# Performance work log

Hardware: AMD Instinct MI355X
Metric: run time of the kernel (lower is better)

Reference implementation:

```python
import jax, jax.numpy as jnp
import numpy as np

EMBED_DIM = 768
HEAD_SIZE = 64

def setup_inputs() -> dict:
    key = jax.random.key(0)
    k1, k2, k3, k4 = jax.random.split(key, 4)
    x = jax.random.normal(k1, (4, 4096, EMBED_DIM), dtype=jnp.float32)
    # nn.Linear(E, H, bias=False) weights, stored as [E, H] for y = x @ W
    scale = 1.0 / np.sqrt(EMBED_DIM)
    Wk = jax.random.uniform(k2, (EMBED_DIM, HEAD_SIZE), jnp.float32, -scale, scale)
    Wq = jax.random.uniform(k3, (EMBED_DIM, HEAD_SIZE), jnp.float32, -scale, scale)
    Wv = jax.random.uniform(k4, (EMBED_DIM, HEAD_SIZE), jnp.float32, -scale, scale)
    return {"x": x, "Wk": Wk, "Wq": Wq, "Wv": Wv}

def reference(x, Wk, Wq, Wv):
    # x: [B, S, E]
    E = x.shape[2]
    K = jnp.einsum("bse,eh->bsh", x, Wk)  # [B, S, H]
    Q = jnp.einsum("bse,eh->bsh", x, Wq)
    V = jnp.einsum("bse,eh->bsh", x, Wv)
    # NOTE: original scales by embedding_dim**0.5, not head_size**0.5
    A = jnp.einsum("bqh,bkh->bqk", Q, K) / jnp.sqrt(jnp.asarray(E, x.dtype))
    A = jax.nn.softmax(A, axis=-1)
    # dropout is inference-mode identity
    return jnp.einsum("bqk,bkh->bqh", A, V)
```

## Files before the change

kernel.cpp:

```cpp
#include <hip/hip_runtime.h>

typedef __attribute__((ext_vector_type(8))) short short8;
typedef __attribute__((ext_vector_type(4))) short short4v;
typedef __attribute__((ext_vector_type(4))) float float4v;

__device__ __forceinline__ short f2bf(float f) {
    union { float f; unsigned u; } v; v.f = f;
    return (short)((v.u + 0x7fffu + ((v.u >> 16) & 1u)) >> 16);
}

__device__ __forceinline__ float fast_exp2(float x) {
#if __has_builtin(__builtin_amdgcn_exp2f)
    return __builtin_amdgcn_exp2f(x);
#else
    return exp2f(x);
#endif
}

__device__ __forceinline__ unsigned cvt_pk_bf16(float lo, float hi) {
    unsigned r;
    asm("v_cvt_pk_bf16_f32 %0, %1, %2" : "=v"(r) : "v"(lo), "v"(hi));
    return r;
}

__global__ void wtrans_kernel(const float* __restrict__ Wk, const float* __restrict__ Wq,
                              const float* __restrict__ Wv, short* __restrict__ Wt3T) {
    int idx = blockIdx.x * 256 + threadIdx.x;
    int p = idx / 12288;
    int rem = idx - p * 12288;
    int kstep = rem / 512;
    int r2 = rem - kstep * 512;
    int lane = r2 >> 3, i = r2 & 7;
    int quad = lane >> 4, l16 = lane & 15;
    int j = p >> 2, nt = p & 3;
    int n = nt * 16 + l16;
    int k = kstep * 32 + quad * 8 + i;
    const float* W = (j == 0) ? Wq : (j == 1 ? Wk : Wv);
    float scale = (j == 0) ? 0.05205877f : 1.0f;
    Wt3T[idx] = f2bf(W[k * 64 + n] * scale);
}

__global__ __launch_bounds__(256, 4) void proj_kernel(
    const float* __restrict__ x, const short* __restrict__ Wt3T,
    short* __restrict__ Qs, short* __restrict__ Kb, short* __restrict__ Vtr)
{
    __shared__ alignas(16) int Abuf[3][256];
    __shared__ alignas(16) short sm[16 * 72];
    const int tid = threadIdx.x;
    const int wave = tid >> 6, lane = tid & 63, quad = lane >> 4, l16 = lane & 15;
    const int m0 = blockIdx.x * 16;
    const int p0 = wave * 3;

    const int xrow = tid >> 4, xcol = (tid & 15) * 2;
    const float* xp = x + (size_t)(m0 + xrow) * 768 + xcol;
    const int aidx = xrow * 16 + (tid & 15);
    const short* wt0 = Wt3T + (size_t)(p0 * 24) * 512 + lane * 8;

    float4v acc[3];
#pragma unroll
    for (int t = 0; t < 3; ++t) acc[t] = (float4v){0.f, 0.f, 0.f, 0.f};

    {
        float2 u = *(const float2*)xp;
        Abuf[0][aidx] = ((unsigned short)f2bf(u.x)) | ((unsigned)f2bf(u.y) << 16);
    }
    short8 Wc0 = *(const short8*)(wt0);
    short8 Wc1 = *(const short8*)(wt0 + 12288);
    short8 Wc2 = *(const short8*)(wt0 + 24576);
    float2 Xn = *(const float2*)(xp + 32);
    __syncthreads();

#pragma unroll
    for (int it = 0; it < 24; ++it) {
        short8 Wn0, Wn1, Wn2;
        float2 Xn2;
        if (it < 23) {
            const short* wn = wt0 + (it + 1) * 512;
            Wn0 = *(const short8*)(wn);
            Wn1 = *(const short8*)(wn + 12288);
            Wn2 = *(const short8*)(wn + 24576);
        }
        if (it < 22) Xn2 = *(const float2*)(xp + (it + 2) * 32);

        short8 a = *(const short8*)((const short*)Abuf[it % 3] + l16 * 32 + quad * 8);
        acc[0] = __builtin_amdgcn_mfma_f32_16x16x32_bf16(a, Wc0, acc[0], 0, 0, 0);
        acc[1] = __builtin_amdgcn_mfma_f32_16x16x32_bf16(a, Wc1, acc[1], 0, 0, 0);
        acc[2] = __builtin_amdgcn_mfma_f32_16x16x32_bf16(a, Wc2, acc[2], 0, 0, 0);

        if (it < 23)
            Abuf[(it + 1) % 3][aidx] = ((unsigned short)f2bf(Xn.x)) | ((unsigned)f2bf(Xn.y) << 16);
        Xn = Xn2;
        Wc0 = Wn0; Wc1 = Wn1; Wc2 = Wn2;
        __syncthreads();
    }

#pragma unroll
    for (int t = 0; t < 3; ++t) {
        const int p = p0 + t, j = p >> 2, nt = p & 3;
        if (j < 2) {
            short* dst = (j == 0) ? Qs : Kb;
#pragma unroll
            for (int r = 0; r < 4; ++r)
                dst[(size_t)(m0 + quad * 4 + r) * 64 + nt * 16 + l16] = f2bf(acc[t][r]);
        } else {
#pragma unroll
            for (int r = 0; r < 4; ++r)
                sm[(quad * 4 + r) * 72 + nt * 16 + l16] = f2bf(acc[t][r]);
        }
    }
    __syncthreads();
    {
        const int h = tid >> 2, si = (tid & 3) * 4;
        const int b = m0 >> 12, s0 = m0 & 4095;
        const int sb = s0 + si;
        const int jb = (sb & ~63) | (sb & 0x23) | ((sb & 0x0C) << 1) | ((sb & 0x10) >> 2);
        short4v tmp;
#pragma unroll
        for (int i = 0; i < 4; ++i) tmp[i] = sm[(si + i) * 72 + h];
        *(short4v*)(Vtr + (size_t)(b * 64 + h) * 4096 + jb) = tmp;
    }
}

__global__ __launch_bounds__(256, 1) void attn_kernel(
    const short* __restrict__ Qs, const short* __restrict__ Kb, const short* __restrict__ Vt,
    float* __restrict__ Opart, float* __restrict__ Ll, int kv_len)
{
    __shared__ alignas(16) short Kl[2][64 * 72];
    __shared__ alignas(16) short Vl[2][64 * 72];

    const int tid = threadIdx.x;
    const int wave = tid >> 6, lane = tid & 63, quad = lane >> 4, l16 = lane & 15;
    const int qt = blockIdx.x, b = blockIdx.y, sp = blockIdx.z;
    const int q0 = qt * 256;
    const int bS = b * 4096;
    const int kv0 = sp * kv_len;

    short8 qb[4][2];
#pragma unroll
    for (int ntq = 0; ntq < 4; ++ntq)
#pragma unroll
        for (int ks = 0; ks < 2; ++ks)
            qb[ntq][ks] = *(const short8*)(Qs + (size_t)(bS + q0 + wave * 64 + ntq * 16 + l16) * 64 + ks * 32 + quad * 8);

    float4v o[4][4];
#pragma unroll
    for (int ntq = 0; ntq < 4; ++ntq)
#pragma unroll
        for (int nt = 0; nt < 4; ++nt) o[ntq][nt] = (float4v){0.f, 0.f, 0.f, 0.f};
    float rs[4] = {0.f, 0.f, 0.f, 0.f};

    const int sr = tid >> 2, sc = (tid & 3) * 16;

    const short* ksrc0 = Kb + (size_t)(bS + kv0 + sr) * 64 + sc;
    const short* vsrc0 = Vt + (size_t)(b * 64 + sr) * 4096 + kv0 + sc;

    const int ntiles = kv_len >> 6;

    short8 kr0 = *(const short8*)ksrc0;
    short8 kr1 = *(const short8*)(ksrc0 + 8);
    short8 vr0 = *(const short8*)vsrc0;
    short8 vr1 = *(const short8*)(vsrc0 + 8);
    *(short8*)&Kl[0][sr * 72 + sc]     = kr0;
    *(short8*)&Kl[0][sr * 72 + sc + 8] = kr1;
    *(short8*)&Vl[0][sr * 72 + sc]     = vr0;
    *(short8*)&Vl[0][sr * 72 + sc + 8] = vr1;
    if (ntiles > 1) {
        const short* kn = ksrc0 + (size_t)4096;
        kr0 = *(const short8*)kn;
        kr1 = *(const short8*)(kn + 8);
        const short* vn = vsrc0 + 64;
        vr0 = *(const short8*)vn;
        vr1 = *(const short8*)(vn + 8);
    }
    __syncthreads();

    for (int t = 0; t < ntiles; ++t) {
        const int c = t & 1;
        const short* klc = &Kl[c][0];
        const short* vlc = &Vl[c][0];

        union { unsigned u[8]; short8 h[2]; } pa0, pa1, pa2, pa3;
#pragma unroll
        for (int mtk = 0; mtk < 4; ++mtk) {
            short8 k0 = *(const short8*)&klc[(mtk * 16 + l16) * 72 + quad * 8];
            short8 k1 = *(const short8*)&klc[(mtk * 16 + l16) * 72 + 32 + quad * 8];
#define QK_NTQ(PA, NTQ)                                                          \
            {                                                                    \
                float4v s = (float4v){0.f, 0.f, 0.f, 0.f};                       \
                __builtin_amdgcn_s_setprio(1);                                   \
                s = __builtin_amdgcn_mfma_f32_16x16x32_bf16(k0, qb[NTQ][0], s, 0, 0, 0); \
                s = __builtin_amdgcn_mfma_f32_16x16x32_bf16(k1, qb[NTQ][1], s, 0, 0, 0); \
                __builtin_amdgcn_s_setprio(0);                                   \
                float e0 = fast_exp2(s[0]), e1 = fast_exp2(s[1]);                \
                float e2 = fast_exp2(s[2]), e3 = fast_exp2(s[3]);                \
                rs[NTQ] += (e0 + e1) + (e2 + e3);                                \
                PA.u[mtk * 2]     = cvt_pk_bf16(e0, e1);                         \
                PA.u[mtk * 2 + 1] = cvt_pk_bf16(e2, e3);                         \
            }
            QK_NTQ(pa0, 0)
            QK_NTQ(pa1, 1)
            QK_NTQ(pa2, 2)
            QK_NTQ(pa3, 3)
#undef QK_NTQ
        }

#pragma unroll
        for (int ks = 0; ks < 2; ++ks) {
            short8 bf[4];
#pragma unroll
            for (int nt = 0; nt < 4; ++nt)
                bf[nt] = *(const short8*)&vlc[(nt * 16 + l16) * 72 + ks * 32 + quad * 8];
            __builtin_amdgcn_s_setprio(1);
#pragma unroll
            for (int nt = 0; nt < 4; ++nt)
                o[0][nt] = __builtin_amdgcn_mfma_f32_16x16x32_bf16(pa0.h[ks], bf[nt], o[0][nt], 0, 0, 0);
#pragma unroll
            for (int nt = 0; nt < 4; ++nt)
                o[1][nt] = __builtin_amdgcn_mfma_f32_16x16x32_bf16(pa1.h[ks], bf[nt], o[1][nt], 0, 0, 0);
#pragma unroll
            for (int nt = 0; nt < 4; ++nt)
                o[2][nt] = __builtin_amdgcn_mfma_f32_16x16x32_bf16(pa2.h[ks], bf[nt], o[2][nt], 0, 0, 0);
#pragma unroll
            for (int nt = 0; nt < 4; ++nt)
                o[3][nt] = __builtin_amdgcn_mfma_f32_16x16x32_bf16(pa3.h[ks], bf[nt], o[3][nt], 0, 0, 0);
            __builtin_amdgcn_s_setprio(0);
        }

        if (t + 1 < ntiles) {
            short* kd = &Kl[c ^ 1][0];
            short* vd = &Vl[c ^ 1][0];
            *(short8*)&kd[sr * 72 + sc]     = kr0;
            *(short8*)&kd[sr * 72 + sc + 8] = kr1;
            *(short8*)&vd[sr * 72 + sc]     = vr0;
            *(short8*)&vd[sr * 72 + sc + 8] = vr1;
        }
        if (t + 2 < ntiles) {
            const short* kn = ksrc0 + (size_t)(t + 2) * 4096;
            kr0 = *(const short8*)kn;
            kr1 = *(const short8*)(kn + 8);
            const short* vn = vsrc0 + (t + 2) * 64;
            vr0 = *(const short8*)vn;
            vr1 = *(const short8*)(vn + 8);
        }
        __syncthreads();
    }

#pragma unroll
    for (int ntq = 0; ntq < 4; ++ntq) {
        rs[ntq] += __shfl_xor(rs[ntq], 16);
        rs[ntq] += __shfl_xor(rs[ntq], 32);
    }

#pragma unroll
    for (int ntq = 0; ntq < 4; ++ntq) {
#pragma unroll
        for (int nt = 0; nt < 4; ++nt)
#pragma unroll
            for (int r = 0; r < 4; ++r) {
                int qrow = q0 + wave * 64 + ntq * 16 + quad * 4 + r;
                Opart[((size_t)sp * 16384 + bS + qrow) * 64 + nt * 16 + l16] = o[ntq][nt][r];
            }
        if (quad == 0)
            Ll[(size_t)sp * 16384 + bS + q0 + wave * 64 + ntq * 16 + l16] = rs[ntq];
    }
}

__global__ void combine_kernel(const float* __restrict__ Opart, const float* __restrict__ Ll,
                               float* __restrict__ out, int nsplit) {
    int idx = blockIdx.x * 256 + threadIdx.x;
    int q = idx >> 6;
    float den = 0.f, num = 0.f;
    for (int s = 0; s < nsplit; ++s) {
        den += Ll[s * 16384 + q];
        num += Opart[(size_t)s * 1048576 + idx];
    }
    out[idx] = num / den;
}

extern "C" void kernel_launch(void* const* d_in, const int* in_sizes, int n_in,
                              void* d_out, int out_size, void* d_ws, size_t ws_size,
                              hipStream_t stream) {
    const float* x  = (const float*)d_in[0];
    const float* Wk = (const float*)d_in[1];
    const float* Wq = (const float*)d_in[2];
    const float* Wv = (const float*)d_in[3];
    float* out = (float*)d_out;

    char* w = (char*)d_ws;
    size_t off = 0;
    auto take = [&](size_t bytes) -> void* {
        void* p = w + off;
        off = (off + bytes + 255) & ~(size_t)255;
        return p;
    };
    short* Qs  = (short*)take((size_t)16384 * 64 * 2);
    short* Kb  = (short*)take((size_t)16384 * 64 * 2);
    short* Vt  = (short*)take((size_t)16384 * 64 * 2);
    short* Wt3 = (short*)take((size_t)3 * 64 * 768 * 2);

    size_t base = off;
    int nsplit = 4;
    while (nsplit > 1) {
        size_t need = base + (((size_t)nsplit * 16384 * 4 + 255) & ~(size_t)255)
                      + (size_t)nsplit * 16384 * 64 * 4 + 512;
        if (need <= ws_size) break;
        nsplit >>= 1;
    }
    float* Ll    = (float*)take((size_t)nsplit * 16384 * 4);
    float* Opart = (float*)take((size_t)nsplit * 16384 * 64 * 4);

    wtrans_kernel<<<576, 256, 0, stream>>>(Wk, Wq, Wv, Wt3);
    proj_kernel<<<1024, 256, 0, stream>>>(x, Wt3, Qs, Kb, Vt);
    dim3 ag(16, 4, nsplit);
    attn_kernel<<<ag, 256, 0, stream>>>(Qs, Kb, Vt, Opart, Ll, 4096 / nsplit);
    combine_kernel<<<4096, 256, 0, stream>>>(Opart, Ll, out, nsplit);
}
```

Baseline: 140.0 us.

## Load K/V fragments directly from global into registers, drop LDS staging

The attention kernel no longer stages K and V tiles through double-buffered shared memory with barriers. Each wave now loads its MFMA operand fragments straight from global memory into registers, prefetching the next tile during compute. Launch bounds are raised to 2 blocks per CU and the KV split count goes from 4 to 8 to add blocks. Each wave now fetches the full K/V tiles itself, so global/L2 traffic rises about fourfold, and the larger partial-output buffer makes the combine step costlier.

```diff
diff --git a/kernel.cpp b/kernel.cpp
--- a/kernel.cpp
+++ b/kernel.cpp
@@ -121,13 +121,10 @@
     }
 }
 
-__global__ __launch_bounds__(256, 1) void attn_kernel(
+__global__ __launch_bounds__(256, 2) void attn_kernel(
     const short* __restrict__ Qs, const short* __restrict__ Kb, const short* __restrict__ Vt,
     float* __restrict__ Opart, float* __restrict__ Ll, int kv_len)
 {
-    __shared__ alignas(16) short Kl[2][64 * 72];
-    __shared__ alignas(16) short Vl[2][64 * 72];
-
     const int tid = threadIdx.x;
     const int wave = tid >> 6, lane = tid & 63, quad = lane >> 4, l16 = lane & 15;
     const int qt = blockIdx.x, b = blockIdx.y, sp = blockIdx.z;
@@ -149,41 +146,29 @@
         for (int nt = 0; nt < 4; ++nt) o[ntq][nt] = (float4v){0.f, 0.f, 0.f, 0.f};
     float rs[4] = {0.f, 0.f, 0.f, 0.f};
 
-    const int sr = tid >> 2, sc = (tid & 3) * 16;
-
-    const short* ksrc0 = Kb + (size_t)(bS + kv0 + sr) * 64 + sc;
-    const short* vsrc0 = Vt + (size_t)(b * 64 + sr) * 4096 + kv0 + sc;
+    const short* kp = Kb + (size_t)(bS + kv0 + l16) * 64 + quad * 8;
+    const short* vp = Vt + (size_t)(b * 64 + l16) * 4096 + kv0 + quad * 8;
 
     const int ntiles = kv_len >> 6;
 
-    short8 kr0 = *(const short8*)ksrc0;
-    short8 kr1 = *(const short8*)(ksrc0 + 8);
-    short8 vr0 = *(const short8*)vsrc0;
-    short8 vr1 = *(const short8*)(vsrc0 + 8);
-    *(short8*)&Kl[0][sr * 72 + sc]     = kr0;
-    *(short8*)&Kl[0][sr * 72 + sc + 8] = kr1;
-    *(short8*)&Vl[0][sr * 72 + sc]     = vr0;
-    *(short8*)&Vl[0][sr * 72 + sc + 8] = vr1;
-    if (ntiles > 1) {
-        const short* kn = ksrc0 + (size_t)4096;
-        kr0 = *(const short8*)kn;
-        kr1 = *(const short8*)(kn + 8);
-        const short* vn = vsrc0 + 64;
-        vr0 = *(const short8*)vn;
-        vr1 = *(const short8*)(vn + 8);
-    }
-    __syncthreads();
+    short8 ka[4], kc[4], va[4], vb[4];
+#pragma unroll
+    for (int mtk = 0; mtk < 4; ++mtk) {
+        ka[mtk] = *(const short8*)(kp + mtk * 1024);
+        kc[mtk] = *(const short8*)(kp + mtk * 1024 + 32);
+    }
+#pragma unroll
+    for (int nt = 0; nt < 4; ++nt) {
+        va[nt] = *(const short8*)(vp + (size_t)nt * 65536);
+        vb[nt] = *(const short8*)(vp + (size_t)nt * 65536 + 32);
+    }
 
     for (int t = 0; t < ntiles; ++t) {
-        const int c = t & 1;
-        const short* klc = &Kl[c][0];
-        const short* vlc = &Vl[c][0];
-
         union { unsigned u[8]; short8 h[2]; } pa0, pa1, pa2, pa3;
 #pragma unroll
         for (int mtk = 0; mtk < 4; ++mtk) {
-            short8 k0 = *(const short8*)&klc[(mtk * 16 + l16) * 72 + quad * 8];
-            short8 k1 = *(const short8*)&klc[(mtk * 16 + l16) * 72 + 32 + quad * 8];
+            short8 k0 = ka[mtk];
+            short8 k1 = kc[mtk];
 #define QK_NTQ(PA, NTQ)                                                          \
             {                                                                    \
                 float4v s = (float4v){0.f, 0.f, 0.f, 0.f};                       \
@@ -204,45 +189,37 @@
 #undef QK_NTQ
         }
 
+        if (t + 1 < ntiles) {
+            const short* kn = kp + (size_t)(t + 1) * 4096;
+#pragma unroll
+            for (int mtk = 0; mtk < 4; ++mtk) {
+                ka[mtk] = *(const short8*)(kn + mtk * 1024);
+                kc[mtk] = *(const short8*)(kn + mtk * 1024 + 32);
+            }
+        }
+
 #pragma unroll
         for (int ks = 0; ks < 2; ++ks) {
-            short8 bf[4];
-#pragma unroll
-            for (int nt = 0; nt < 4; ++nt)
-                bf[nt] = *(const short8*)&vlc[(nt * 16 + l16) * 72 + ks * 32 + quad * 8];
             __builtin_amdgcn_s_setprio(1);
 #pragma unroll
-            for (int nt = 0; nt < 4; ++nt)
-                o[0][nt] = __builtin_amdgcn_mfma_f32_16x16x32_bf16(pa0.h[ks], bf[nt], o[0][nt], 0, 0, 0);
-#pragma unroll
-            for (int nt = 0; nt < 4; ++nt)
-                o[1][nt] = __builtin_amdgcn_mfma_f32_16x16x32_bf16(pa1.h[ks], bf[nt], o[1][nt], 0, 0, 0);
-#pragma unroll
-            for (int nt = 0; nt < 4; ++nt)
-                o[2][nt] = __builtin_amdgcn_mfma_f32_16x16x32_bf16(pa2.h[ks], bf[nt], o[2][nt], 0, 0, 0);
-#pragma unroll
-            for (int nt = 0; nt < 4; ++nt)
-                o[3][nt] = __builtin_amdgcn_mfma_f32_16x16x32_bf16(pa3.h[ks], bf[nt], o[3][nt], 0, 0, 0);
+            for (int nt = 0; nt < 4; ++nt) {
+                short8 bf = (ks == 0) ? va[nt] : vb[nt];
+                o[0][nt] = __builtin_amdgcn_mfma_f32_16x16x32_bf16(pa0.h[ks], bf, o[0][nt], 0, 0, 0);
+                o[1][nt] = __builtin_amdgcn_mfma_f32_16x16x32_bf16(pa1.h[ks], bf, o[1][nt], 0, 0, 0);
+                o[2][nt] = __builtin_amdgcn_mfma_f32_16x16x32_bf16(pa2.h[ks], bf, o[2][nt], 0, 0, 0);
+                o[3][nt] = __builtin_amdgcn_mfma_f32_16x16x32_bf16(pa3.h[ks], bf, o[3][nt], 0, 0, 0);
+            }
             __builtin_amdgcn_s_setprio(0);
         }
 
         if (t + 1 < ntiles) {
-            short* kd = &Kl[c ^ 1][0];
-            short* vd = &Vl[c ^ 1][0];
-            *(short8*)&kd[sr * 72 + sc]     = kr0;
-            *(short8*)&kd[sr * 72 + sc + 8] = kr1;
-            *(short8*)&vd[sr * 72 + sc]     = vr0;
-            *(short8*)&vd[sr * 72 + sc + 8] = vr1;
-        }
-        if (t + 2 < ntiles) {
-            const short* kn = ksrc0 + (size_t)(t + 2) * 4096;
-            kr0 = *(const short8*)kn;
-            kr1 = *(const short8*)(kn + 8);
-            const short* vn = vsrc0 + (t + 2) * 64;
-            vr0 = *(const short8*)vn;
-            vr1 = *(const short8*)(vn + 8);
-        }
-        __syncthreads();
+            const short* vn = vp + (t + 1) * 64;
+#pragma unroll
+            for (int nt = 0; nt < 4; ++nt) {
+                va[nt] = *(const short8*)(vn + (size_t)nt * 65536);
+                vb[nt] = *(const short8*)(vn + (size_t)nt * 65536 + 32);
+            }
+        }
     }
 
 #pragma unroll
@@ -299,7 +276,7 @@
     short* Wt3 = (short*)take((size_t)3 * 64 * 768 * 2);
 
     size_t base = off;
-    int nsplit = 4;
+    int nsplit = 8;
     while (nsplit > 1) {
         size_t need = base + (((size_t)nsplit * 16384 * 4 + 255) & ~(size_t)255)
                       + (size_t)nsplit * 16384 * 64 * 4 + 512;
```

Result: slower. 172.5 us (+23.2%).

## Single-buffer attention LDS, allow two blocks per CU, and double KV splits

Applied to the files above, without the earlier changes.

The attention kernel drops its double-buffered K/V shared-memory tiles in favor of a single buffer with two barriers per tile. Global prefetch of the next tile into registers is kept. Launch bounds now allow two blocks per CU, and the KV dimension is split eight ways instead of four, which gives 512 blocks instead of 256 to fill the GPU. The trade-off is an extra barrier per tile, tighter register limits, and more partial output to write and combine.

```diff
diff --git a/kernel.cpp b/kernel.cpp
--- a/kernel.cpp
+++ b/kernel.cpp
@@ -121,12 +121,12 @@
     }
 }
 
-__global__ __launch_bounds__(256, 1) void attn_kernel(
+__global__ __launch_bounds__(256, 2) void attn_kernel(
     const short* __restrict__ Qs, const short* __restrict__ Kb, const short* __restrict__ Vt,
     float* __restrict__ Opart, float* __restrict__ Ll, int kv_len)
 {
-    __shared__ alignas(16) short Kl[2][64 * 72];
-    __shared__ alignas(16) short Vl[2][64 * 72];
+    __shared__ alignas(16) short Kl[64 * 72];
+    __shared__ alignas(16) short Vl[64 * 72];
 
     const int tid = threadIdx.x;
     const int wave = tid >> 6, lane = tid & 63, quad = lane >> 4, l16 = lane & 15;
@@ -154,36 +154,34 @@
     const short* ksrc0 = Kb + (size_t)(bS + kv0 + sr) * 64 + sc;
     const short* vsrc0 = Vt + (size_t)(b * 64 + sr) * 4096 + kv0 + sc;
 
-    const int ntiles = kv_len >> 6;
-
     short8 kr0 = *(const short8*)ksrc0;
     short8 kr1 = *(const short8*)(ksrc0 + 8);
     short8 vr0 = *(const short8*)vsrc0;
     short8 vr1 = *(const short8*)(vsrc0 + 8);
-    *(short8*)&Kl[0][sr * 72 + sc]     = kr0;
-    *(short8*)&Kl[0][sr * 72 + sc + 8] = kr1;
-    *(short8*)&Vl[0][sr * 72 + sc]     = vr0;
-    *(short8*)&Vl[0][sr * 72 + sc + 8] = vr1;
-    if (ntiles > 1) {
-        const short* kn = ksrc0 + (size_t)4096;
-        kr0 = *(const short8*)kn;
-        kr1 = *(const short8*)(kn + 8);
-        const short* vn = vsrc0 + 64;
-        vr0 = *(const short8*)vn;
-        vr1 = *(const short8*)(vn + 8);
-    }
-    __syncthreads();
-
+
+    const int ntiles = kv_len >> 6;
     for (int t = 0; t < ntiles; ++t) {
-        const int c = t & 1;
-        const short* klc = &Kl[c][0];
-        const short* vlc = &Vl[c][0];
+        __syncthreads();
+        *(short8*)&Kl[sr * 72 + sc]     = kr0;
+        *(short8*)&Kl[sr * 72 + sc + 8] = kr1;
+        *(short8*)&Vl[sr * 72 + sc]     = vr0;
+        *(short8*)&Vl[sr * 72 + sc + 8] = vr1;
+        __syncthreads();
+
+        if (t + 1 < ntiles) {
+            const short* kn = ksrc0 + (size_t)(t + 1) * 4096;
+            kr0 = *(const short8*)kn;
+            kr1 = *(const short8*)(kn + 8);
+            const short* vn = vsrc0 + (t + 1) * 64;
+            vr0 = *(const short8*)vn;
+            vr1 = *(const short8*)(vn + 8);
+        }
 
         union { unsigned u[8]; short8 h[2]; } pa0, pa1, pa2, pa3;
 #pragma unroll
         for (int mtk = 0; mtk < 4; ++mtk) {
-            short8 k0 = *(const short8*)&klc[(mtk * 16 + l16) * 72 + quad * 8];
-            short8 k1 = *(const short8*)&klc[(mtk * 16 + l16) * 72 + 32 + quad * 8];
+            short8 k0 = *(const short8*)&Kl[(mtk * 16 + l16) * 72 + quad * 8];
+            short8 k1 = *(const short8*)&Kl[(mtk * 16 + l16) * 72 + 32 + quad * 8];
 #define QK_NTQ(PA, NTQ)                                                          \
             {                                                                    \
                 float4v s = (float4v){0.f, 0.f, 0.f, 0.f};                       \
@@ -209,7 +207,7 @@
             short8 bf[4];
 #pragma unroll
             for (int nt = 0; nt < 4; ++nt)
-                bf[nt] = *(const short8*)&vlc[(nt * 16 + l16) * 72 + ks * 32 + quad * 8];
+                bf[nt] = *(const short8*)&Vl[(nt * 16 + l16) * 72 + ks * 32 + quad * 8];
             __builtin_amdgcn_s_setprio(1);
 #pragma unroll
             for (int nt = 0; nt < 4; ++nt)
@@ -225,24 +223,6 @@
                 o[3][nt] = __builtin_amdgcn_mfma_f32_16x16x32_bf16(pa3.h[ks], bf[nt], o[3][nt], 0, 0, 0);
             __builtin_amdgcn_s_setprio(0);
         }
-
-        if (t + 1 < ntiles) {
-            short* kd = &Kl[c ^ 1][0];
-            short* vd = &Vl[c ^ 1][0];
-            *(short8*)&kd[sr * 72 + sc]     = kr0;
-            *(short8*)&kd[sr * 72 + sc + 8] = kr1;
-            *(short8*)&vd[sr * 72 + sc]     = vr0;
-            *(short8*)&vd[sr * 72 + sc + 8] = vr1;
-        }
-        if (t + 2 < ntiles) {
-            const short* kn = ksrc0 + (size_t)(t + 2) * 4096;
-            kr0 = *(const short8*)kn;
-            kr1 = *(const short8*)(kn + 8);
-            const short* vn = vsrc0 + (t + 2) * 64;
-            vr0 = *(const short8*)vn;
-            vr1 = *(const short8*)(vn + 8);
-        }
-        __syncthreads();
     }
 
 #pragma unroll
@@ -299,7 +279,7 @@
     short* Wt3 = (short*)take((size_t)3 * 64 * 768 * 2);
 
     size_t base = off;
-    int nsplit = 4;
+    int nsplit = 8;
     while (nsplit > 1) {
         size_t need = base + (((size_t)nsplit * 16384 * 4 + 255) & ~(size_t)255)
                       + (size_t)nsplit * 16384 * 64 * 4 + 512;
```

Result: faster. 136.7 us (-2.3%).
